# Performance work log

Hardware: AMD Instinct MI355X
Metric: run time of the kernel (lower is better)

Reference implementation:

```python
import jax, jax.numpy as jnp
import numpy as np

B, S, D, H = 32, 1024, 256, 256


def setup_inputs() -> dict:
    key = jax.random.key(0)
    ks = jax.random.split(key, 7)
    s_in = 1.0 / np.sqrt(D)
    s_h = 1.0 / np.sqrt(H)
    x = jax.random.normal(ks[0], (B, S, D), dtype=jnp.float32)
    # gate order: i, f, g, o stacked along last dim -> 4H
    W_fwd = jax.random.uniform(ks[1], (D, 4 * H), dtype=jnp.float32, minval=-s_in, maxval=s_in)
    U_fwd = jax.random.uniform(ks[2], (H, 4 * H), dtype=jnp.float32, minval=-s_h, maxval=s_h)
    b_fwd = jax.random.uniform(ks[3], (4 * H,), dtype=jnp.float32, minval=-s_in, maxval=s_in)
    W_rev = jax.random.uniform(ks[4], (D, 4 * H), dtype=jnp.float32, minval=-s_in, maxval=s_in)
    U_rev = jax.random.uniform(ks[5], (H, 4 * H), dtype=jnp.float32, minval=-s_h, maxval=s_h)
    b_rev = jax.random.uniform(ks[6], (4 * H,), dtype=jnp.float32, minval=-s_in, maxval=s_in)
    return {"x": x, "W_fwd": W_fwd, "U_fwd": U_fwd, "b_fwd": b_fwd,
            "W_rev": W_rev, "U_rev": U_rev, "b_rev": b_rev}


def _lstm_scan(x, W, U, b):
    # x: [B, S, D] -> outputs h over time: [B, S, H]
    hdim = U.shape[0]
    # precompute input projection for all steps: [S, B, 4H]
    xW = jnp.einsum('bsd,dg->sbg', x, W) + b

    def step(carry, xw_t):
        h, c = carry
        gates = xw_t + h @ U  # [B, 4H]
        i_t = jax.nn.sigmoid(gates[:, 0 * hdim:1 * hdim])
        f_t = jax.nn.sigmoid(gates[:, 1 * hdim:2 * hdim])
        g_t = jnp.tanh(gates[:, 2 * hdim:3 * hdim])
        o_t = jax.nn.sigmoid(gates[:, 3 * hdim:4 * hdim])
        c_t = f_t * c + i_t * g_t
        h_t = o_t * jnp.tanh(c_t)
        return (h_t, c_t), h_t

    bsz = x.shape[0]
    h0 = jnp.zeros((bsz, hdim), dtype=x.dtype)
    c0 = jnp.zeros((bsz, hdim), dtype=x.dtype)
    _, hs = jax.lax.scan(step, (h0, c0), xW)
    return jnp.transpose(hs, (1, 0, 2))  # [B, S, H]


def reference(x, W_fwd, U_fwd, b_fwd, W_rev, U_rev, b_rev):
    out_f = _lstm_scan(x, W_fwd, U_fwd, b_fwd)
    out_r = _lstm_scan(x[:, ::-1, :], W_rev, U_rev, b_rev)[:, ::-1, :]
    return jnp.concatenate([out_f, out_r], axis=2)  # [B, S, 2H]
```

## Files before the change

kernel.cpp:

```cpp
#include <hip/hip_runtime.h>
#include <hip/hip_bf16.h>

typedef _Float16 f16;
typedef _Float16 half8 __attribute__((ext_vector_type(8)));
typedef float f32x4 __attribute__((ext_vector_type(4)));


__global__ void prep_uq_kernel(const float* __restrict__ Uf, const float* __restrict__ Ur,
                               unsigned int* __restrict__ UQ, float* __restrict__ Uscale)
{
    int idx = blockIdx.x * 256 + threadIdx.x;
    if (idx >= 2048) return;
    int dir = idx >> 10, j = idx & 1023;
    const float* U = dir ? Ur : Uf;
    float m = 0.f;
    for (int k = 0; k < 256; ++k) m = fmaxf(m, fabsf(U[k * 1024 + j]));
    float sinv = (m > 0.f) ? 127.f / m : 0.f;
    for (int kk = 0; kk < 64; ++kk) {
        unsigned int w = 0;
        #pragma unroll
        for (int e = 0; e < 4; ++e) {
            float v = U[(kk * 4 + e) * 1024 + j];
            int q = __float2int_rn(v * sinv);
            w |= ((unsigned int)(q & 0xff)) << (8 * e);
        }
        UQ[(((size_t)dir * 1024 + j) * 16 + (kk >> 2)) * 4 + (kk & 3)] = w;
    }
    Uscale[idx] = m / (127.f * 127.f);
}

__global__ __launch_bounds__(256) void proj_gemm_kernel(
    const float* __restrict__ x, const float* __restrict__ Wf, const float* __restrict__ Wr,
    const float* __restrict__ bfw, const float* __restrict__ brw, f16* __restrict__ G)
{
    const int nt = blockIdx.x;
    const int mt = blockIdx.y;
    const int m0 = mt * 128, n0 = nt * 128;
    const int dir = n0 >> 10, nin0 = n0 & 1023;
    const float* W   = dir ? Wr : Wf;
    const float* bia = dir ? brw : bfw;
    __shared__ f16 Asm[128][40];
    __shared__ f16 Bsm[128][40];
    const int t = threadIdx.x;
    const int lane = t & 63, wave = t >> 6;
    const int wr = wave >> 1, wc = wave & 1;
    f32x4 acc[4][4] = {};
    for (int k0 = 0; k0 < 256; k0 += 32) {
        #pragma unroll
        for (int e = 0; e < 16; ++e) {
            int idx = e * 256 + t;
            int r = idx >> 5, kk = idx & 31;
            Asm[r][kk] = (f16)x[(size_t)(m0 + r) * 256 + (k0 + kk)];
        }
        #pragma unroll
        for (int e = 0; e < 16; ++e) {
            int idx = e * 256 + t;
            int col = idx & 127, kr = idx >> 7;
            Bsm[col][kr] = (f16)W[(size_t)(k0 + kr) * 1024 + (nin0 + col)];
        }
        __syncthreads();
        const int l15 = lane & 15, kb = (lane >> 4) * 8;
        half8 af[4], bfr[4];
        #pragma unroll
        for (int fr = 0; fr < 4; ++fr) af[fr]  = *(const half8*)&Asm[wr * 64 + fr * 16 + l15][kb];
        #pragma unroll
        for (int fc = 0; fc < 4; ++fc) bfr[fc] = *(const half8*)&Bsm[wc * 64 + fc * 16 + l15][kb];
        #pragma unroll
        for (int fr = 0; fr < 4; ++fr)
            #pragma unroll
            for (int fc = 0; fc < 4; ++fc)
                acc[fr][fc] = __builtin_amdgcn_mfma_f32_16x16x32_f16(af[fr], bfr[fc], acc[fr][fc], 0, 0, 0);
        __syncthreads();
    }
    const int row4 = (lane >> 4) * 4, c15 = lane & 15;
    #pragma unroll
    for (int fr = 0; fr < 4; ++fr)
        #pragma unroll
        for (int fc = 0; fc < 4; ++fc) {
            int rbase = m0 + wr * 64 + fr * 16 + row4;
            int cidx  = n0 + wc * 64 + fc * 16 + c15;
            float bv = bia[cidx & 1023];
            #pragma unroll
            for (int i = 0; i < 4; ++i)
                G[(size_t)(rbase + i) * 2048 + cidx] = (f16)(acc[fr][fc][i] + bv);
        }
}

__device__ __forceinline__ int dot4i8(unsigned int a, unsigned int b, int c) {
#if __has_builtin(__builtin_amdgcn_sdot4)
    return __builtin_amdgcn_sdot4(a, b, c, false);
#else
    c += (int)(signed char)(a)       * (int)(signed char)(b);
    c += (int)(signed char)(a >> 8)  * (int)(signed char)(b >> 8);
    c += (int)(signed char)(a >> 16) * (int)(signed char)(b >> 16);
    c += (int)(signed char)(a >> 24) * (int)(signed char)(b >> 24);
    return c;
#endif
}

__device__ __forceinline__ float tanh_fast(float x) {
    float e = __expf(2.f * x);
    return 1.f - 2.f / (e + 1.f);
}

__global__
__attribute__((amdgpu_flat_work_group_size(1024, 1024)))
__attribute__((amdgpu_waves_per_eu(4, 4)))
void scan_kernel(
    const f16* __restrict__ G, const unsigned int* __restrict__ UQ,
    const float* __restrict__ Uscale, float* __restrict__ out)
{
    const int wg = blockIdx.x;
    const int dir = wg >> 5, b = wg & 31;
    const int g = threadIdx.x;
    __shared__ __align__(16) unsigned int hq[64];
    __shared__ float preact[1024];

    const uint4* up = (const uint4*)(UQ + (((size_t)dir * 1024 + g) << 6));
    uint4 ureg[16];
    #pragma unroll
    for (int kkk = 0; kkk < 16; ++kkk)
        asm volatile("global_load_dwordx4 %0, %1, off offset:%2"
                     : "=v"(ureg[kkk]) : "v"(up), "i"(kkk * 16));
    asm volatile("s_waitcnt vmcnt(0)" ::: "memory");
    __builtin_amdgcn_sched_barrier(0);

    const float usc = Uscale[dir * 1024 + g];

    float c_state = 0.f;
    if (g < 64) hq[g] = 0u;
    const long stride = dir ? -2048 : 2048;
    const f16* gp = G + (size_t)b * 1024 * 2048 + dir * 1024 + g
                      + (dir ? (size_t)1023 * 2048 : 0);
    float* outp = out + (size_t)b * 1024 * 512 + dir * 256 + g;
    f16 xw_c = *gp;
    __syncthreads();

    const uint4* hp4 = (const uint4*)hq;

    for (int t = 0; t < 1024; ++t) {
        const f16* gn = gp + ((t < 1023) ? stride : 0);
        f16 xw_n = *gn;

        int i0 = 0, i1 = 0, i2 = 0, i3 = 0;
        #pragma unroll
        for (int ch = 0; ch < 4; ++ch) {
            uint4 ha = hp4[ch * 4 + 0];
            uint4 hb = hp4[ch * 4 + 1];
            uint4 hc = hp4[ch * 4 + 2];
            uint4 hd = hp4[ch * 4 + 3];
            i0 = dot4i8(ureg[ch * 4 + 0].x, ha.x, i0);
            i1 = dot4i8(ureg[ch * 4 + 0].y, ha.y, i1);
            i2 = dot4i8(ureg[ch * 4 + 0].z, ha.z, i2);
            i3 = dot4i8(ureg[ch * 4 + 0].w, ha.w, i3);
            i0 = dot4i8(ureg[ch * 4 + 1].x, hb.x, i0);
            i1 = dot4i8(ureg[ch * 4 + 1].y, hb.y, i1);
            i2 = dot4i8(ureg[ch * 4 + 1].z, hb.z, i2);
            i3 = dot4i8(ureg[ch * 4 + 1].w, hb.w, i3);
            i0 = dot4i8(ureg[ch * 4 + 2].x, hc.x, i0);
            i1 = dot4i8(ureg[ch * 4 + 2].y, hc.y, i1);
            i2 = dot4i8(ureg[ch * 4 + 2].z, hc.z, i2);
            i3 = dot4i8(ureg[ch * 4 + 2].w, hc.w, i3);
            i0 = dot4i8(ureg[ch * 4 + 3].x, hd.x, i0);
            i1 = dot4i8(ureg[ch * 4 + 3].y, hd.y, i1);
            i2 = dot4i8(ureg[ch * 4 + 3].z, hd.z, i2);
            i3 = dot4i8(ureg[ch * 4 + 3].w, hd.w, i3);
            __builtin_amdgcn_sched_barrier(0);
        }
        int iacc = (i0 + i1) + (i2 + i3);
        preact[g] = (float)xw_c + (float)iacc * usc;
        __syncthreads();

        if (g < 256) {
            float pi = preact[g];
            float pf = preact[256 + g];
            float pg = preact[512 + g];
            float po = preact[768 + g];
            float ig = 1.f / (1.f + __expf(-pi));
            float fg = 1.f / (1.f + __expf(-pf));
            float gg = tanh_fast(pg);
            float og = 1.f / (1.f + __expf(-po));
            c_state = fg * c_state + ig * gg;
            float h = og * tanh_fast(c_state);
            int s = dir ? (1023 - t) : t;
            outp[(size_t)s * 512] = h;
            int iq = __float2int_rn(h * 127.f);
            ((signed char*)hq)[g] = (signed char)iq;
        }
        __syncthreads();
        xw_c = xw_n;
        gp = gn;
    }
}

extern "C" void kernel_launch(void* const* d_in, const int* in_sizes, int n_in,
                              void* d_out, int out_size, void* d_ws, size_t ws_size,
                              hipStream_t stream) {
    const float* x  = (const float*)d_in[0];
    const float* Wf = (const float*)d_in[1];
    const float* Uf = (const float*)d_in[2];
    const float* bf = (const float*)d_in[3];
    const float* Wr = (const float*)d_in[4];
    const float* Ur = (const float*)d_in[5];
    const float* br = (const float*)d_in[6];
    float* out = (float*)d_out;

    char* ws = (char*)d_ws;
    unsigned int* UQ = (unsigned int*)ws;
    float* Uscale    = (float*)(ws + (size_t)512 * 1024);
    f16* G           = (f16*)(ws + (size_t)1024 * 1024);

    prep_uq_kernel<<<8, 256, 0, stream>>>(Uf, Ur, UQ, Uscale);
    dim3 gg(16, 256);
    proj_gemm_kernel<<<gg, 256, 0, stream>>>(x, Wf, Wr, bf, br, G);
    scan_kernel<<<64, 1024, 0, stream>>>(G, UQ, Uscale, out);
}
```

Measured before the change: 1.132 ms.

## Split recurrent matvec between int8 MFMA waves and sdot4 threads in scan

The scan kernel now splits the 1024 gate columns in two. The first 512 columns are computed by 8 waves using int8 16x16x64 MFMA on U fragments held in registers, taken from a newly prepared MFMA-friendly layout. The remaining 512 are computed per thread with sdot4 as before. Input-projection loads and the bias add move into the 256 gate threads, which prefetch all four gates for the next step. This aims to shorten the per-step matvec latency, at the cost of extra prep work and a second weight layout. The MFMA path wastes rows, since only row 0 of A is meaningful.

```diff
diff --git a/kernel.cpp b/kernel.cpp
--- a/kernel.cpp
+++ b/kernel.cpp
@@ -4,27 +4,51 @@
 typedef _Float16 f16;
 typedef _Float16 half8 __attribute__((ext_vector_type(8)));
 typedef float f32x4 __attribute__((ext_vector_type(4)));
+typedef int i32x4 __attribute__((ext_vector_type(4)));
 
 
 __global__ void prep_uq_kernel(const float* __restrict__ Uf, const float* __restrict__ Ur,
-                               unsigned int* __restrict__ UQ, float* __restrict__ Uscale)
+                               unsigned int* __restrict__ UQd, unsigned int* __restrict__ UQm,
+                               float* __restrict__ Uscale)
 {
     int idx = blockIdx.x * 256 + threadIdx.x;
     if (idx >= 2048) return;
-    int dir = idx >> 10, j = idx & 1023;
+    int dir = idx >> 10, c = idx & 1023;
     const float* U = dir ? Ur : Uf;
     float m = 0.f;
-    for (int k = 0; k < 256; ++k) m = fmaxf(m, fabsf(U[k * 1024 + j]));
+    for (int k = 0; k < 256; ++k) m = fmaxf(m, fabsf(U[k * 1024 + c]));
     float sinv = (m > 0.f) ? 127.f / m : 0.f;
     for (int kk = 0; kk < 64; ++kk) {
         unsigned int w = 0;
         #pragma unroll
         for (int e = 0; e < 4; ++e) {
-            float v = U[(kk * 4 + e) * 1024 + j];
-            int q = __float2int_rn(v * sinv);
+            int q = __float2int_rn(U[(kk * 4 + e) * 1024 + c] * sinv);
             w |= ((unsigned int)(q & 0xff)) << (8 * e);
         }
-        UQ[(((size_t)dir * 1024 + j) * 16 + (kk >> 2)) * 4 + (kk & 3)] = w;
+        UQd[((size_t)(dir * 1024 + c)) * 64 + kk] = w;
+    }
+    if (c < 512) {
+        int tile = c >> 4, colr = c & 15;
+        uint4* UQm4 = (uint4*)UQm;
+        for (int ks = 0; ks < 4; ++ks) {
+            #pragma unroll
+            for (int kg = 0; kg < 4; ++kg) {
+                unsigned int w[4];
+                #pragma unroll
+                for (int d = 0; d < 4; ++d) {
+                    unsigned int wd = 0;
+                    #pragma unroll
+                    for (int e = 0; e < 4; ++e) {
+                        int k = ks * 64 + kg * 16 + d * 4 + e;
+                        int q = __float2int_rn(U[k * 1024 + c] * sinv);
+                        wd |= ((unsigned int)(q & 0xff)) << (8 * e);
+                    }
+                    w[d] = wd;
+                }
+                UQm4[((size_t)((dir * 32 + tile) * 4 + ks)) * 64 + kg * 16 + colr] =
+                    make_uint4(w[0], w[1], w[2], w[3]);
+            }
+        }
     }
     Uscale[idx] = m / (127.f * 127.f);
 }
@@ -105,91 +129,144 @@
 
 __global__
 __attribute__((amdgpu_flat_work_group_size(1024, 1024)))
-__attribute__((amdgpu_waves_per_eu(4, 4)))
 void scan_kernel(
-    const f16* __restrict__ G, const unsigned int* __restrict__ UQ,
-    const float* __restrict__ Uscale, float* __restrict__ out)
+    const f16* __restrict__ G, const unsigned int* __restrict__ UQd,
+    const unsigned int* __restrict__ UQm, const float* __restrict__ Uscale,
+    float* __restrict__ out)
 {
     const int wg = blockIdx.x;
     const int dir = wg >> 5, b = wg & 31;
-    const int g = threadIdx.x;
+    const int tid = threadIdx.x;
+    const int wave = tid >> 6, lane = tid & 63;
+    const bool is_dot  = (tid >= 512);
+    const bool is_gate = (tid >= 512 && tid < 768);
+    const int gc = tid & 255;
+
     __shared__ __align__(16) unsigned int hq[64];
-    __shared__ float preact[1024];
-
-    const uint4* up = (const uint4*)(UQ + (((size_t)dir * 1024 + g) << 6));
+    __shared__ float pre[1024];
+
+    if (tid < 64) hq[tid] = 0u;
+
+    const f16* Grow = G + (size_t)b * 1024 * 2048 + dir * 1024 + gc;
+    float* outp = out + (size_t)b * 1024 * 512 + dir * 256 + gc;
+    float xwc0 = 0.f, xwc1 = 0.f, xwc2 = 0.f, xwc3 = 0.f;
+    float c_state = 0.f;
+    const int s0 = dir ? 1023 : 0;
+    if (is_gate) {
+        xwc0 = (float)Grow[(size_t)s0 * 2048 + 0];
+        xwc1 = (float)Grow[(size_t)s0 * 2048 + 256];
+        xwc2 = (float)Grow[(size_t)s0 * 2048 + 512];
+        xwc3 = (float)Grow[(size_t)s0 * 2048 + 768];
+    }
+
     uint4 ureg[16];
-    #pragma unroll
-    for (int kkk = 0; kkk < 16; ++kkk)
-        asm volatile("global_load_dwordx4 %0, %1, off offset:%2"
-                     : "=v"(ureg[kkk]) : "v"(up), "i"(kkk * 16));
-    asm volatile("s_waitcnt vmcnt(0)" ::: "memory");
-    __builtin_amdgcn_sched_barrier(0);
-
-    const float usc = Uscale[dir * 1024 + g];
-
-    float c_state = 0.f;
-    if (g < 64) hq[g] = 0u;
-    const long stride = dir ? -2048 : 2048;
-    const f16* gp = G + (size_t)b * 1024 * 2048 + dir * 1024 + g
-                      + (dir ? (size_t)1023 * 2048 : 0);
-    float* outp = out + (size_t)b * 1024 * 512 + dir * 256 + g;
-    f16 xw_c = *gp;
+    float usc = 0.f;
+    i32x4 uf[4][4];
+    float usc4[4] = {0.f, 0.f, 0.f, 0.f};
+
+    if (is_dot) {
+        const uint4* up = (const uint4*)(UQd + ((size_t)(dir * 1024 + tid)) * 64);
+        #pragma unroll
+        for (int kkk = 0; kkk < 16; ++kkk)
+            asm volatile("global_load_dwordx4 %0, %1, off offset:%2"
+                         : "=v"(ureg[kkk]) : "v"(up), "i"(kkk * 16));
+        asm volatile("s_waitcnt vmcnt(0)" ::: "memory");
+        __builtin_amdgcn_sched_barrier(0);
+        usc = Uscale[dir * 1024 + tid];
+    } else {
+        const i32x4* UQm4 = (const i32x4*)UQm;
+        #pragma unroll
+        for (int tau = 0; tau < 4; ++tau)
+            #pragma unroll
+            for (int ks = 0; ks < 4; ++ks)
+                uf[tau][ks] = UQm4[((size_t)((dir * 32 + wave * 4 + tau) * 4 + ks)) * 64 + lane];
+        if (lane < 16) {
+            #pragma unroll
+            for (int tau = 0; tau < 4; ++tau)
+                usc4[tau] = Uscale[dir * 1024 + wave * 64 + tau * 16 + lane];
+        }
+    }
     __syncthreads();
 
     const uint4* hp4 = (const uint4*)hq;
+    const char* hqb = (const char*)hq;
 
     for (int t = 0; t < 1024; ++t) {
-        const f16* gn = gp + ((t < 1023) ? stride : 0);
-        f16 xw_n = *gn;
-
-        int i0 = 0, i1 = 0, i2 = 0, i3 = 0;
-        #pragma unroll
-        for (int ch = 0; ch < 4; ++ch) {
-            uint4 ha = hp4[ch * 4 + 0];
-            uint4 hb = hp4[ch * 4 + 1];
-            uint4 hc = hp4[ch * 4 + 2];
-            uint4 hd = hp4[ch * 4 + 3];
-            i0 = dot4i8(ureg[ch * 4 + 0].x, ha.x, i0);
-            i1 = dot4i8(ureg[ch * 4 + 0].y, ha.y, i1);
-            i2 = dot4i8(ureg[ch * 4 + 0].z, ha.z, i2);
-            i3 = dot4i8(ureg[ch * 4 + 0].w, ha.w, i3);
-            i0 = dot4i8(ureg[ch * 4 + 1].x, hb.x, i0);
-            i1 = dot4i8(ureg[ch * 4 + 1].y, hb.y, i1);
-            i2 = dot4i8(ureg[ch * 4 + 1].z, hb.z, i2);
-            i3 = dot4i8(ureg[ch * 4 + 1].w, hb.w, i3);
-            i0 = dot4i8(ureg[ch * 4 + 2].x, hc.x, i0);
-            i1 = dot4i8(ureg[ch * 4 + 2].y, hc.y, i1);
-            i2 = dot4i8(ureg[ch * 4 + 2].z, hc.z, i2);
-            i3 = dot4i8(ureg[ch * 4 + 2].w, hc.w, i3);
-            i0 = dot4i8(ureg[ch * 4 + 3].x, hd.x, i0);
-            i1 = dot4i8(ureg[ch * 4 + 3].y, hd.y, i1);
-            i2 = dot4i8(ureg[ch * 4 + 3].z, hd.z, i2);
-            i3 = dot4i8(ureg[ch * 4 + 3].w, hd.w, i3);
-            __builtin_amdgcn_sched_barrier(0);
-        }
-        int iacc = (i0 + i1) + (i2 + i3);
-        preact[g] = (float)xw_c + (float)iacc * usc;
-        __syncthreads();
-
-        if (g < 256) {
-            float pi = preact[g];
-            float pf = preact[256 + g];
-            float pg = preact[512 + g];
-            float po = preact[768 + g];
+        const int s  = dir ? (1023 - t) : t;
+        const int tn = (t < 1023) ? (t + 1) : t;
+        const int sn = dir ? (1023 - tn) : tn;
+
+        f16 xn0, xn1, xn2, xn3;
+        if (is_gate) {
+            xn0 = Grow[(size_t)sn * 2048 + 0];
+            xn1 = Grow[(size_t)sn * 2048 + 256];
+            xn2 = Grow[(size_t)sn * 2048 + 512];
+            xn3 = Grow[(size_t)sn * 2048 + 768];
+        }
+
+        if (is_dot) {
+            int i0 = 0, i1 = 0, i2 = 0, i3 = 0;
+            #pragma unroll
+            for (int ch = 0; ch < 4; ++ch) {
+                uint4 ha = hp4[ch * 4 + 0];
+                uint4 hb = hp4[ch * 4 + 1];
+                uint4 hc = hp4[ch * 4 + 2];
+                uint4 hd = hp4[ch * 4 + 3];
+                i0 = dot4i8(ureg[ch * 4 + 0].x, ha.x, i0);
+                i1 = dot4i8(ureg[ch * 4 + 0].y, ha.y, i1);
+                i2 = dot4i8(ureg[ch * 4 + 0].z, ha.z, i2);
+                i3 = dot4i8(ureg[ch * 4 + 0].w, ha.w, i3);
+                i0 = dot4i8(ureg[ch * 4 + 1].x, hb.x, i0);
+                i1 = dot4i8(ureg[ch * 4 + 1].y, hb.y, i1);
+                i2 = dot4i8(ureg[ch * 4 + 1].z, hb.z, i2);
+                i3 = dot4i8(ureg[ch * 4 + 1].w, hb.w, i3);
+                i0 = dot4i8(ureg[ch * 4 + 2].x, hc.x, i0);
+                i1 = dot4i8(ureg[ch * 4 + 2].y, hc.y, i1);
+                i2 = dot4i8(ureg[ch * 4 + 2].z, hc.z, i2);
+                i3 = dot4i8(ureg[ch * 4 + 2].w, hc.w, i3);
+                i0 = dot4i8(ureg[ch * 4 + 3].x, hd.x, i0);
+                i1 = dot4i8(ureg[ch * 4 + 3].y, hd.y, i1);
+                i2 = dot4i8(ureg[ch * 4 + 3].z, hd.z, i2);
+                i3 = dot4i8(ureg[ch * 4 + 3].w, hd.w, i3);
+                __builtin_amdgcn_sched_barrier(0);
+            }
+            int iacc = (i0 + i1) + (i2 + i3);
+            pre[tid] = (float)iacc * usc;
+        } else {
+            i32x4 acc0 = {0,0,0,0}, acc1 = {0,0,0,0}, acc2 = {0,0,0,0}, acc3 = {0,0,0,0};
+            #pragma unroll
+            for (int ks = 0; ks < 4; ++ks) {
+                i32x4 a = *(const i32x4*)(hqb + ks * 64 + ((lane >> 4) << 4));
+                acc0 = __builtin_amdgcn_mfma_i32_16x16x64_i8(a, uf[0][ks], acc0, 0, 0, 0);
+                acc1 = __builtin_amdgcn_mfma_i32_16x16x64_i8(a, uf[1][ks], acc1, 0, 0, 0);
+                acc2 = __builtin_amdgcn_mfma_i32_16x16x64_i8(a, uf[2][ks], acc2, 0, 0, 0);
+                acc3 = __builtin_amdgcn_mfma_i32_16x16x64_i8(a, uf[3][ks], acc3, 0, 0, 0);
+            }
+            if (lane < 16) {
+                pre[wave * 64 +  0 + lane] = (float)acc0[0] * usc4[0];
+                pre[wave * 64 + 16 + lane] = (float)acc1[0] * usc4[1];
+                pre[wave * 64 + 32 + lane] = (float)acc2[0] * usc4[2];
+                pre[wave * 64 + 48 + lane] = (float)acc3[0] * usc4[3];
+            }
+        }
+        __syncthreads();
+
+        if (is_gate) {
+            float pi = pre[gc      ] + xwc0;
+            float pf = pre[gc + 256] + xwc1;
+            float pg = pre[gc + 512] + xwc2;
+            float po = pre[gc + 768] + xwc3;
             float ig = 1.f / (1.f + __expf(-pi));
             float fg = 1.f / (1.f + __expf(-pf));
             float gg = tanh_fast(pg);
             float og = 1.f / (1.f + __expf(-po));
             c_state = fg * c_state + ig * gg;
             float h = og * tanh_fast(c_state);
-            int s = dir ? (1023 - t) : t;
             outp[(size_t)s * 512] = h;
-            int iq = __float2int_rn(h * 127.f);
-            ((signed char*)hq)[g] = (signed char)iq;
-        }
-        __syncthreads();
-        xw_c = xw_n;
-        gp = gn;
+            ((signed char*)hq)[gc] = (signed char)__float2int_rn(h * 127.f);
+            xwc0 = (float)xn0; xwc1 = (float)xn1; xwc2 = (float)xn2; xwc3 = (float)xn3;
+        }
+        __syncthreads();
     }
 }
 
@@ -206,12 +283,13 @@
     float* out = (float*)d_out;
 
     char* ws = (char*)d_ws;
-    unsigned int* UQ = (unsigned int*)ws;
-    float* Uscale    = (float*)(ws + (size_t)512 * 1024);
-    f16* G           = (f16*)(ws + (size_t)1024 * 1024);
-
-    prep_uq_kernel<<<8, 256, 0, stream>>>(Uf, Ur, UQ, Uscale);
+    unsigned int* UQd = (unsigned int*)ws;
+    float* Uscale     = (float*)(ws + (size_t)512 * 1024);
+    unsigned int* UQm = (unsigned int*)(ws + (size_t)768 * 1024);
+    f16* G            = (f16*)(ws + (size_t)1024 * 1024);
+
+    prep_uq_kernel<<<8, 256, 0, stream>>>(Uf, Ur, UQd, UQm, Uscale);
     dim3 gg(16, 256);
     proj_gemm_kernel<<<gg, 256, 0, stream>>>(x, Wf, Wr, bf, br, G);
-    scan_kernel<<<64, 1024, 0, stream>>>(G, UQ, Uscale, out);
-}
+    scan_kernel<<<64, 1024, 0, stream>>>(G, UQd, UQm, Uscale, out);
+}
```

Result: slower. 3.580 ms (+216.4%).
